# Performance work log

Hardware: AMD Instinct MI355X
Metric: run time of the kernel (lower is better)

The kernel has to match this reference:

```python
import jax, jax.numpy as jnp
import numpy as np

BN_EPS = 1e-5
DIST_EPS = 1e-8


def setup_inputs() -> dict:
    key = jax.random.key(0)
    ks = jax.random.split(key, 8)
    B, N, M = 8, 8192, 2048
    C1, C2 = 128, 256
    Cin = C1 + C2  # 384
    H = 256
    return {
        "xyz1": jax.random.normal(ks[0], (B, N, 3), dtype=jnp.float32),
        "xyz2": jax.random.normal(ks[1], (B, M, 3), dtype=jnp.float32),
        "points1": jax.random.normal(ks[2], (B, N, C1), dtype=jnp.float32),
        "points2": jax.random.normal(ks[3], (B, M, C2), dtype=jnp.float32),
        "W1": jax.random.normal(ks[4], (H, Cin), dtype=jnp.float32) * 0.05,
        "b1": jnp.zeros((H,), dtype=jnp.float32),
        "gamma1": jnp.ones((H,), dtype=jnp.float32),
        "beta1": jnp.zeros((H,), dtype=jnp.float32),
        "W2": jax.random.normal(ks[5], (H, H), dtype=jnp.float32) * 0.05,
        "b2": jnp.zeros((H,), dtype=jnp.float32),
        "gamma2": jnp.ones((H,), dtype=jnp.float32),
        "beta2": jnp.zeros((H,), dtype=jnp.float32),
    }


def _interpolate(xyz1, xyz2, points2):
    # squared distances (B,N,M) via the bmm expansion, as in square_distance
    d = (jnp.sum(xyz1 * xyz1, -1)[:, :, None]
         + jnp.sum(xyz2 * xyz2, -1)[:, None, :]
         - 2.0 * jnp.einsum("bnc,bmc->bnm", xyz1, xyz2))
    neg, idx = jax.lax.top_k(-d, 3)          # 3 smallest distances
    dists = -neg                              # (B,N,3)
    recip = 1.0 / (dists + DIST_EPS)
    w = recip / jnp.sum(recip, -1, keepdims=True)  # (B,N,3)
    gathered = jax.vmap(lambda p, i: p[i])(points2, idx)  # (B,N,3,C2)
    return jnp.einsum("bnkc,bnk->bnc", gathered, w)


def _conv_bn_relu(x, W, b, gamma, beta):
    # pointwise conv1d: (B,N,Cin) x (Cout,Cin) -> (B,N,Cout)
    y = jnp.einsum("bnc,oc->bno", x, W) + b
    mean = jnp.mean(y, axis=(0, 1))           # BatchNorm1d (training-mode batch stats)
    var = jnp.var(y, axis=(0, 1))
    y = (y - mean) * jax.lax.rsqrt(var + BN_EPS) * gamma + beta
    return jax.nn.relu(y)


def reference(xyz1, xyz2, points1, points2, W1, b1, gamma1, beta1, W2, b2, gamma2, beta2):
    interp = _interpolate(xyz1, xyz2, points2)          # (B,N,C2)
    x = jnp.concatenate([points1, interp], axis=-1)     # (B,N,C1+C2)
    x = _conv_bn_relu(x, W1, b1, gamma1, beta1)
    x = _conv_bn_relu(x, W2, b2, gamma2, beta2)
    return x  # (B,N,mlp[-1])
```

## Files before the change

kernel.cpp:

```cpp
#include <hip/hip_runtime.h>
#include <hip/hip_bf16.h>
#include <stdint.h>

#define B_SZ  8
#define N_Q   8192
#define M_PT  2048
#define C1    128
#define C2    256
#define CIN   384
#define H_OUT 256
#define R_TOT 65536

#define NCH   8
#define CHM   (M_PT / NCH)
#define QPB   32

typedef __bf16 bf16x8 __attribute__((ext_vector_type(8)));
typedef __bf16 bf16x4 __attribute__((ext_vector_type(4)));
typedef __bf16 bf16x2 __attribute__((ext_vector_type(2)));
typedef float  f32x4  __attribute__((ext_vector_type(4)));

__device__ __forceinline__ void async_copy16(const void* g, void* l) {
    __builtin_amdgcn_global_load_lds(
        (const __attribute__((address_space(1))) unsigned int*)g,
        (__attribute__((address_space(3))) unsigned int*)l,
        16, 0, 0);
}

__global__ __launch_bounds__(256) void f2bf2(const float* __restrict__ a, int na,
                                             const float* __restrict__ b, int nb,
                                             __bf16* __restrict__ oa,
                                             __bf16* __restrict__ ob) {
    int i = blockIdx.x * 256 + threadIdx.x;
    if (i < na)            oa[i] = (__bf16)a[i];
    else if (i - na < nb)  ob[i - na] = (__bf16)b[i - na];
}

__global__ __launch_bounds__(256) void knn_partial(
    const float* __restrict__ xyz1, const float* __restrict__ xyz2,
    float* __restrict__ cand_d, int* __restrict__ cand_i) {
    __shared__ float4 pos[CHM];

    const int tid = threadIdx.x;
    const int c   = blockIdx.x & (NCH - 1);
    const int qb  = (blockIdx.x >> 3) & 31;
    const int b   = blockIdx.x >> 8;

    {
        const float* x2 = xyz2 + ((size_t)b * M_PT + c * CHM) * 3;
        float x = x2[tid * 3], y = x2[tid * 3 + 1], z = x2[tid * 3 + 2];
        pos[tid] = make_float4(x, y, z, x * x + y * y + z * z);
    }
    __syncthreads();

    const int q = b * N_Q + qb * 256 + tid;
    const float* q1 = xyz1 + (size_t)q * 3;
    float x1 = q1[0], y1 = q1[1], z1 = q1[2];
    float n1 = x1 * x1 + y1 * y1 + z1 * z1;
    float d0 = 3.4e38f, d1 = 3.4e38f, d2 = 3.4e38f;
    int   i0 = 0, i1 = 0, i2 = 0;
    const int jb = c * CHM;
#pragma unroll 8
    for (int j = 0; j < CHM; ++j) {
        float4 p  = pos[j];
        float dot = fmaf(x1, p.x, fmaf(y1, p.y, z1 * p.z));
        float d   = fmaf(-2.f, dot, n1 + p.w);
        const int jj = jb + j;
        const bool c2 = d < d2, c1 = d < d1, c0 = d < d0;
        const int ni2 = c1 ? i1 : (c2 ? jj : i2);
        const int ni1 = c0 ? i0 : (c1 ? jj : i1);
        const int ni0 = c0 ? jj : i0;
        const float nd2 = fminf(fmaxf(d, d1), d2);
        const float nd1 = __builtin_amdgcn_fmed3f(d, d0, d1);
        const float nd0 = fminf(d, d0);
        i2 = ni2; i1 = ni1; i0 = ni0;
        d2 = nd2; d1 = nd1; d0 = nd0;
    }
    const size_t base = (size_t)q * (NCH * 3) + c * 3;
    cand_d[base] = d0; cand_d[base + 1] = d1; cand_d[base + 2] = d2;
    cand_i[base] = i0; cand_i[base + 1] = i1; cand_i[base + 2] = i2;
}

__global__ __launch_bounds__(256) void interp_gather(
    const float* __restrict__ p1,     const float* __restrict__ p2,
    const float* __restrict__ cand_d, const int* __restrict__ cand_i,
    __bf16* __restrict__ xb) {
    __shared__ float wgt[QPB * 3];
    __shared__ int   ids[QPB * 3];

    const int tid = threadIdx.x;
    const int b   = blockIdx.x >> 8;
    const int q0  = (blockIdx.x & 255) * QPB;

    if (tid < QPB) {
        const int q = b * N_Q + q0 + tid;
        const float* cd = cand_d + (size_t)q * (NCH * 3);
        const int*   ci = cand_i + (size_t)q * (NCH * 3);
        float d0 = 3.4e38f, d1 = 3.4e38f, d2 = 3.4e38f;
        int   i0 = 0, i1 = 0, i2 = 0;
#pragma unroll
        for (int t = 0; t < NCH * 3; ++t) {
            float d = cd[t]; int i = ci[t];
            const bool c2 = d < d2, c1 = d < d1, c0 = d < d0;
            const int ni2 = c1 ? i1 : (c2 ? i : i2);
            const int ni1 = c0 ? i0 : (c1 ? i : i1);
            const int ni0 = c0 ? i : i0;
            const float nd2 = fminf(fmaxf(d, d1), d2);
            const float nd1 = __builtin_amdgcn_fmed3f(d, d0, d1);
            const float nd0 = fminf(d, d0);
            i2 = ni2; i1 = ni1; i0 = ni0;
            d2 = nd2; d1 = nd1; d0 = nd0;
        }
        float r0 = 1.f / (d0 + 1e-8f), r1 = 1.f / (d1 + 1e-8f), r2 = 1.f / (d2 + 1e-8f);
        float rs = 1.f / (r0 + r1 + r2);
        wgt[tid * 3] = r0 * rs; wgt[tid * 3 + 1] = r1 * rs; wgt[tid * 3 + 2] = r2 * rs;
        ids[tid * 3] = i0;      ids[tid * 3 + 1] = i1;      ids[tid * 3 + 2] = i2;
    }
    __syncthreads();

    const int wave = tid >> 6, lane = tid & 63;
    const float* p2b = p2 + (size_t)b * M_PT * C2;
    const float* p1b = p1 + (size_t)(b * N_Q + q0) * C1;
    __bf16* outp = xb + (size_t)(b * N_Q + q0) * CIN;
    for (int qq = wave; qq < QPB; qq += 4) {
        float w0 = wgt[qq * 3], w1 = wgt[qq * 3 + 1], w2 = wgt[qq * 3 + 2];
        int   j0 = ids[qq * 3], j1 = ids[qq * 3 + 1], j2 = ids[qq * 3 + 2];
        const float4* ra = (const float4*)(p2b + (size_t)j0 * C2);
        const float4* rb = (const float4*)(p2b + (size_t)j1 * C2);
        const float4* rc = (const float4*)(p2b + (size_t)j2 * C2);
        float4 va = ra[lane], vb = rb[lane], vc = rc[lane];
        bf16x4 o;
        o[0] = (__bf16)(w0 * va.x + w1 * vb.x + w2 * vc.x);
        o[1] = (__bf16)(w0 * va.y + w1 * vb.y + w2 * vc.y);
        o[2] = (__bf16)(w0 * va.z + w1 * vb.z + w2 * vc.z);
        o[3] = (__bf16)(w0 * va.w + w1 * vb.w + w2 * vc.w);
        *(bf16x4*)(outp + (size_t)qq * CIN + C1 + lane * 4) = o;
        float2 pv = ((const float2*)(p1b + (size_t)qq * C1))[lane];
        bf16x2 o2; o2[0] = (__bf16)pv.x; o2[1] = (__bf16)pv.y;
        *(bf16x2*)(outp + (size_t)qq * CIN + lane * 2) = o2;
    }
}

template <int K, bool OUT_BF16>
__global__ __launch_bounds__(256, 2) void gemm_bt(const __bf16* __restrict__ A,
                                                  const __bf16* __restrict__ Bw,
                                                  void* __restrict__ Cout,
                                                  float* __restrict__ partS,
                                                  float* __restrict__ partQ) {
    __shared__ __attribute__((aligned(16))) __bf16 As[128 * 32];
    __shared__ __attribute__((aligned(16))) __bf16 Bs[128 * 32];
    const int tid  = threadIdx.x;
    const int wave = tid >> 6, lane = tid & 63;
    const int wm = wave >> 1, wn = wave & 1;
    const int quad = lane >> 4, r16 = lane & 15;
    const int bx = blockIdx.x & 1, by = blockIdx.x >> 1;
    const int l4 = lane >> 2, lk = (lane & 3) * 8;

    f32x4 acc[4][4] = {};

    const __bf16* gA = A  + (size_t)(by * 128 + wave * 32 + l4) * K + lk;
    const __bf16* gB = Bw + (size_t)(bx * 128 + wave * 32 + l4) * K + lk;
    char* lA = (char*)As + wave * 2048;
    char* lB = (char*)Bs + wave * 2048;

    for (int k0 = 0; k0 < K; k0 += 32) {
        async_copy16(gA + k0,                  lA);
        async_copy16(gA + k0 + (size_t)16 * K, lA + 1024);
        async_copy16(gB + k0,                  lB);
        async_copy16(gB + k0 + (size_t)16 * K, lB + 1024);
        __syncthreads();

        bf16x8 af[4], bf[4];
#pragma unroll
        for (int t = 0; t < 4; ++t)
            af[t] = *(const bf16x8*)(As + (wm * 64 + t * 16 + r16) * 32 + quad * 8);
#pragma unroll
        for (int u = 0; u < 4; ++u)
            bf[u] = *(const bf16x8*)(Bs + (wn * 64 + u * 16 + r16) * 32 + quad * 8);
#pragma unroll
        for (int t = 0; t < 4; ++t)
#pragma unroll
            for (int u = 0; u < 4; ++u)
                acc[t][u] = __builtin_amdgcn_mfma_f32_16x16x32_bf16(af[t], bf[u], acc[t][u], 0, 0, 0);
        __syncthreads();
    }

#pragma unroll
    for (int t = 0; t < 4; ++t) {
#pragma unroll
        for (int u = 0; u < 4; ++u) {
            const int col = bx * 128 + wn * 64 + u * 16 + r16;
#pragma unroll
            for (int r = 0; r < 4; ++r) {
                const int row = by * 128 + wm * 64 + t * 16 + quad * 4 + r;
                if (OUT_BF16)
                    ((__bf16*)Cout)[(size_t)row * H_OUT + col] = (__bf16)acc[t][u][r];
                else
                    ((float*)Cout)[(size_t)row * H_OUT + col] = acc[t][u][r];
            }
        }
    }

    float* redS = (float*)As;
    float* redQ = ((float*)As) + 1024;
    const int slot = wm * 4 + quad;
#pragma unroll
    for (int u = 0; u < 4; ++u) {
        float s = 0.f, qq = 0.f;
#pragma unroll
        for (int t = 0; t < 4; ++t)
#pragma unroll
            for (int r = 0; r < 4; ++r) { float v = acc[t][u][r]; s += v; qq = fmaf(v, v, qq); }
        const int col = wn * 64 + u * 16 + r16;
        redS[col * 8 + slot] = s;
        redQ[col * 8 + slot] = qq;
    }
    __syncthreads();
    if (tid < 128) {
        float s = 0.f, qq = 0.f;
#pragma unroll
        for (int k = 0; k < 8; ++k) { s += redS[tid * 8 + k]; qq += redQ[tid * 8 + k]; }
        partS[(size_t)blockIdx.x * 128 + tid] = s;
        partQ[(size_t)blockIdx.x * 128 + tid] = qq;
    }
}

__global__ __launch_bounds__(256) void bn_finalize(const float* __restrict__ pS,
                                                   const float* __restrict__ pQ,
                                                   const float* __restrict__ gamma,
                                                   const float* __restrict__ beta,
                                                   float* __restrict__ sc,
                                                   float* __restrict__ sh) {
    const int c = threadIdx.x;
    const int half = c >> 7, lo = c & 127;
    float s = 0.f, q = 0.f;
    for (int p = 0; p < 512; ++p) {
        const size_t off = (size_t)(p * 2 + half) * 128 + lo;
        s += pS[off];
        q += pQ[off];
    }
    const float inv = 1.f / (float)R_TOT;
    float mean = s * inv;
    float var  = q * inv - mean * mean;
    float a    = gamma[c] * rsqrtf(var + 1e-5f);
    sc[c] = a;
    sh[c] = beta[c] - mean * a;
}

__global__ __launch_bounds__(256) void apply_bf16(__bf16* __restrict__ y,
                                                  const float* __restrict__ sc,
                                                  const float* __restrict__ sh) {
    __shared__ float scs[256], shs[256];
    scs[threadIdx.x] = sc[threadIdx.x];
    shs[threadIdx.x] = sh[threadIdx.x];
    __syncthreads();
    size_t i = ((size_t)blockIdx.x * 256 + threadIdx.x) * 8;
    int c0 = (int)(i & 255);
    bf16x8 v = *(const bf16x8*)(y + i);
#pragma unroll
    for (int e = 0; e < 8; ++e) {
        float f = fmaf((float)v[e], scs[c0 + e], shs[c0 + e]);
        v[e] = (__bf16)fmaxf(f, 0.f);
    }
    *(bf16x8*)(y + i) = v;
}

__global__ __launch_bounds__(256) void apply_f32(float* __restrict__ y,
                                                 const float* __restrict__ sc,
                                                 const float* __restrict__ sh) {
    __shared__ float scs[256], shs[256];
    scs[threadIdx.x] = sc[threadIdx.x];
    shs[threadIdx.x] = sh[threadIdx.x];
    __syncthreads();
    size_t i = ((size_t)blockIdx.x * 256 + threadIdx.x) * 4;
    int c0 = (int)(i & 255);
    float4 v = *(const float4*)(y + i);
    v.x = fmaxf(fmaf(v.x, scs[c0 + 0], shs[c0 + 0]), 0.f);
    v.y = fmaxf(fmaf(v.y, scs[c0 + 1], shs[c0 + 1]), 0.f);
    v.z = fmaxf(fmaf(v.z, scs[c0 + 2], shs[c0 + 2]), 0.f);
    v.w = fmaxf(fmaf(v.w, scs[c0 + 3], shs[c0 + 3]), 0.f);
    *(float4*)(y + i) = v;
}

extern "C" void kernel_launch(void* const* d_in, const int* in_sizes, int n_in,
                              void* d_out, int out_size, void* d_ws, size_t ws_size,
                              hipStream_t stream) {
    const float* xyz1 = (const float*)d_in[0];
    const float* xyz2 = (const float*)d_in[1];
    const float* p1   = (const float*)d_in[2];
    const float* p2   = (const float*)d_in[3];
    const float* W1   = (const float*)d_in[4];
    const float* g1   = (const float*)d_in[6];
    const float* be1  = (const float*)d_in[7];
    const float* W2   = (const float*)d_in[8];
    const float* g2   = (const float*)d_in[10];
    const float* be2  = (const float*)d_in[11];
    float* out = (float*)d_out;

    char* ws = (char*)d_ws;
    __bf16* xb     = (__bf16*)(ws);
    __bf16* y1b    = (__bf16*)(ws + 50331648);
    float*  cand_d = (float*) (ws + 50331648);
    int*    cand_i = (int*)   (ws + 56623104);
    __bf16* wb1    = (__bf16*)(ws + 83886080);
    __bf16* wb2    = (__bf16*)(ws + 84082688);
    float*  sc1    = (float*) (ws + 84213760);
    float*  sh1    = sc1 + 256;
    float*  sc2    = sc1 + 512;
    float*  sh2    = sc1 + 768;

    float* partS1 = (float*)d_out;
    float* partQ1 = partS1 + 131072;
    float* partS2 = (float*)ws;
    float* partQ2 = partS2 + 131072;

    f2bf2<<<640, 256, 0, stream>>>(W1, H_OUT * CIN, W2, H_OUT * H_OUT, wb1, wb2);

    knn_partial<<<B_SZ * 32 * NCH, 256, 0, stream>>>(xyz1, xyz2, cand_d, cand_i);
    interp_gather<<<R_TOT / QPB, 256, 0, stream>>>(p1, p2, cand_d, cand_i, xb);

    gemm_bt<CIN, true><<<1024, 256, 0, stream>>>(xb, wb1, (void*)y1b, partS1, partQ1);
    bn_finalize<<<1, 256, 0, stream>>>(partS1, partQ1, g1, be1, sc1, sh1);
    apply_bf16<<<8192, 256, 0, stream>>>(y1b, sc1, sh1);

    gemm_bt<H_OUT, false><<<1024, 256, 0, stream>>>(y1b, wb2, (void*)out, partS2, partQ2);
    bn_finalize<<<1, 256, 0, stream>>>(partS2, partQ2, g2, be2, sc2, sh2);
    apply_f32<<<16384, 256, 0, stream>>>(out, sc2, sh2);
}
```

Baseline: 320.8 us.

## Split KNN into value-only top-3 pass, merge, and index-recovery pass; parallelize BN finalize

Replaces the single KNN pass that tracked distances and indices together with three kernels. The first keeps only the three smallest partial distances per chunk, dropping the query norm and using fmed3 with no index selects. A merge kernel then combines the chunks and computes the interpolation weights, and a second pass recomputes distances to recover indices by exact float equality. BN finalize also moves from a single-block serial loop to one block per channel with a tree reduction. The cost is a second full distance sweep, plus index recovery that relies on bitwise-identical recomputed distances and resolves ties to the lowest index.

```diff
diff --git a/kernel.cpp b/kernel.cpp
--- a/kernel.cpp
+++ b/kernel.cpp
@@ -36,54 +36,105 @@
     else if (i - na < nb)  ob[i - na] = (__bf16)b[i - na];
 }
 
-__global__ __launch_bounds__(256) void knn_partial(
+__global__ __launch_bounds__(256) void knn_vals(
     const float* __restrict__ xyz1, const float* __restrict__ xyz2,
-    float* __restrict__ cand_d, int* __restrict__ cand_i) {
+    float4* __restrict__ vals4) {
     __shared__ float4 pos[CHM];
-
     const int tid = threadIdx.x;
     const int c   = blockIdx.x & (NCH - 1);
     const int qb  = (blockIdx.x >> 3) & 31;
     const int b   = blockIdx.x >> 8;
-
     {
         const float* x2 = xyz2 + ((size_t)b * M_PT + c * CHM) * 3;
         float x = x2[tid * 3], y = x2[tid * 3 + 1], z = x2[tid * 3 + 2];
-        pos[tid] = make_float4(x, y, z, x * x + y * y + z * z);
+        pos[tid] = make_float4(-2.f * x, -2.f * y, -2.f * z,
+                               fmaf(x, x, fmaf(y, y, z * z)));
     }
     __syncthreads();
 
     const int q = b * N_Q + qb * 256 + tid;
     const float* q1 = xyz1 + (size_t)q * 3;
     float x1 = q1[0], y1 = q1[1], z1 = q1[2];
-    float n1 = x1 * x1 + y1 * y1 + z1 * z1;
-    float d0 = 3.4e38f, d1 = 3.4e38f, d2 = 3.4e38f;
-    int   i0 = 0, i1 = 0, i2 = 0;
-    const int jb = c * CHM;
+    float v0 = 3.4e38f, v1 = 3.4e38f, v2 = 3.4e38f;
 #pragma unroll 8
     for (int j = 0; j < CHM; ++j) {
-        float4 p  = pos[j];
-        float dot = fmaf(x1, p.x, fmaf(y1, p.y, z1 * p.z));
-        float d   = fmaf(-2.f, dot, n1 + p.w);
-        const int jj = jb + j;
-        const bool c2 = d < d2, c1 = d < d1, c0 = d < d0;
-        const int ni2 = c1 ? i1 : (c2 ? jj : i2);
-        const int ni1 = c0 ? i0 : (c1 ? jj : i1);
-        const int ni0 = c0 ? jj : i0;
-        const float nd2 = fminf(fmaxf(d, d1), d2);
-        const float nd1 = __builtin_amdgcn_fmed3f(d, d0, d1);
-        const float nd0 = fminf(d, d0);
-        i2 = ni2; i1 = ni1; i0 = ni0;
-        d2 = nd2; d1 = nd1; d0 = nd0;
-    }
-    const size_t base = (size_t)q * (NCH * 3) + c * 3;
-    cand_d[base] = d0; cand_d[base + 1] = d1; cand_d[base + 2] = d2;
-    cand_i[base] = i0; cand_i[base + 1] = i1; cand_i[base + 2] = i2;
+        float4 p = pos[j];
+        float d  = fmaf(p.x, x1, fmaf(p.y, y1, fmaf(p.z, z1, p.w)));
+        float n0 = fminf(d, v0);
+        float n1 = __builtin_amdgcn_fmed3f(d, v0, v1);
+        float n2 = __builtin_amdgcn_fmed3f(d, v1, v2);
+        v0 = n0; v1 = n1; v2 = n2;
+    }
+    vals4[(size_t)c * R_TOT + q] = make_float4(v0, v1, v2, 0.f);
+}
+
+__global__ __launch_bounds__(256) void knn_merge(
+    const float4* __restrict__ vals4, const float* __restrict__ xyz1,
+    float4* __restrict__ v4, float4* __restrict__ w4) {
+    const int q = blockIdx.x * 256 + threadIdx.x;
+    float v0 = 3.4e38f, v1 = 3.4e38f, v2 = 3.4e38f;
+#pragma unroll
+    for (int c = 0; c < NCH; ++c) {
+        float4 t = vals4[(size_t)c * R_TOT + q];
+#pragma unroll
+        for (int k = 0; k < 3; ++k) {
+            float d  = (k == 0) ? t.x : (k == 1) ? t.y : t.z;
+            float n0 = fminf(d, v0);
+            float n1 = __builtin_amdgcn_fmed3f(d, v0, v1);
+            float n2 = __builtin_amdgcn_fmed3f(d, v1, v2);
+            v0 = n0; v1 = n1; v2 = n2;
+        }
+    }
+    const float* q1 = xyz1 + (size_t)q * 3;
+    float x1 = q1[0], y1 = q1[1], z1 = q1[2];
+    float n1q = fmaf(x1, x1, fmaf(y1, y1, z1 * z1));
+    float r0 = 1.f / ((v0 + n1q) + 1e-8f);
+    float r1 = 1.f / ((v1 + n1q) + 1e-8f);
+    float r2 = 1.f / ((v2 + n1q) + 1e-8f);
+    float rs = 1.f / (r0 + r1 + r2);
+    v4[q] = make_float4(v0, v1, v2, 0.f);
+    w4[q] = make_float4(r0 * rs, r1 * rs, r2 * rs, 0.f);
+}
+
+__global__ __launch_bounds__(256) void knn_recover(
+    const float* __restrict__ xyz1, const float* __restrict__ xyz2,
+    const float4* __restrict__ v4, int4* __restrict__ ci4) {
+    __shared__ float4 pos[CHM];
+    const int tid = threadIdx.x;
+    const int c   = blockIdx.x & (NCH - 1);
+    const int qb  = (blockIdx.x >> 3) & 31;
+    const int b   = blockIdx.x >> 8;
+    {
+        const float* x2 = xyz2 + ((size_t)b * M_PT + c * CHM) * 3;
+        float x = x2[tid * 3], y = x2[tid * 3 + 1], z = x2[tid * 3 + 2];
+        pos[tid] = make_float4(-2.f * x, -2.f * y, -2.f * z,
+                               fmaf(x, x, fmaf(y, y, z * z)));
+    }
+    __syncthreads();
+
+    const int q = b * N_Q + qb * 256 + tid;
+    const float* q1 = xyz1 + (size_t)q * 3;
+    float x1 = q1[0], y1 = q1[1], z1 = q1[2];
+    const float4 vv = v4[q];
+    int i0 = 0x7fffffff, i1 = 0x7fffffff, i2 = 0x7fffffff;
+    const int jb = c * CHM;
+#pragma unroll 4
+    for (int j = 0; j < CHM; ++j) {
+        float4 p = pos[j];
+        float d  = fmaf(p.x, x1, fmaf(p.y, y1, fmaf(p.z, z1, p.w)));
+        if (d <= vv.z) {
+            const int jj = jb + j;
+            i0 = min(i0, (d == vv.x) ? jj : 0x7fffffff);
+            i1 = min(i1, (d == vv.y) ? jj : 0x7fffffff);
+            i2 = min(i2, (d == vv.z) ? jj : 0x7fffffff);
+        }
+    }
+    ci4[(size_t)c * R_TOT + q] = make_int4(i0, i1, i2, 0);
 }
 
 __global__ __launch_bounds__(256) void interp_gather(
-    const float* __restrict__ p1,     const float* __restrict__ p2,
-    const float* __restrict__ cand_d, const int* __restrict__ cand_i,
+    const float* __restrict__ p1,  const float* __restrict__ p2,
+    const int4* __restrict__ ci4,  const float4* __restrict__ w4,
     __bf16* __restrict__ xb) {
     __shared__ float wgt[QPB * 3];
     __shared__ int   ids[QPB * 3];
@@ -94,27 +145,15 @@
 
     if (tid < QPB) {
         const int q = b * N_Q + q0 + tid;
-        const float* cd = cand_d + (size_t)q * (NCH * 3);
-        const int*   ci = cand_i + (size_t)q * (NCH * 3);
-        float d0 = 3.4e38f, d1 = 3.4e38f, d2 = 3.4e38f;
-        int   i0 = 0, i1 = 0, i2 = 0;
-#pragma unroll
-        for (int t = 0; t < NCH * 3; ++t) {
-            float d = cd[t]; int i = ci[t];
-            const bool c2 = d < d2, c1 = d < d1, c0 = d < d0;
-            const int ni2 = c1 ? i1 : (c2 ? i : i2);
-            const int ni1 = c0 ? i0 : (c1 ? i : i1);
-            const int ni0 = c0 ? i : i0;
-            const float nd2 = fminf(fmaxf(d, d1), d2);
-            const float nd1 = __builtin_amdgcn_fmed3f(d, d0, d1);
-            const float nd0 = fminf(d, d0);
-            i2 = ni2; i1 = ni1; i0 = ni0;
-            d2 = nd2; d1 = nd1; d0 = nd0;
+        int i0 = 0x7fffffff, i1 = 0x7fffffff, i2 = 0x7fffffff;
+#pragma unroll
+        for (int c = 0; c < NCH; ++c) {
+            int4 t = ci4[(size_t)c * R_TOT + q];
+            i0 = min(i0, t.x); i1 = min(i1, t.y); i2 = min(i2, t.z);
         }
-        float r0 = 1.f / (d0 + 1e-8f), r1 = 1.f / (d1 + 1e-8f), r2 = 1.f / (d2 + 1e-8f);
-        float rs = 1.f / (r0 + r1 + r2);
-        wgt[tid * 3] = r0 * rs; wgt[tid * 3 + 1] = r1 * rs; wgt[tid * 3 + 2] = r2 * rs;
-        ids[tid * 3] = i0;      ids[tid * 3 + 1] = i1;      ids[tid * 3 + 2] = i2;
+        float4 w = w4[q];
+        wgt[tid * 3] = w.x; wgt[tid * 3 + 1] = w.y; wgt[tid * 3 + 2] = w.z;
+        ids[tid * 3] = i0;  ids[tid * 3 + 1] = i1;  ids[tid * 3 + 2] = i2;
     }
     __syncthreads();
 
@@ -231,20 +270,27 @@
                                                    const float* __restrict__ beta,
                                                    float* __restrict__ sc,
                                                    float* __restrict__ sh) {
-    const int c = threadIdx.x;
+    __shared__ float rs[256], rq[256];
+    const int c = blockIdx.x;
+    const int t = threadIdx.x;
     const int half = c >> 7, lo = c & 127;
-    float s = 0.f, q = 0.f;
-    for (int p = 0; p < 512; ++p) {
-        const size_t off = (size_t)(p * 2 + half) * 128 + lo;
-        s += pS[off];
-        q += pQ[off];
-    }
-    const float inv = 1.f / (float)R_TOT;
-    float mean = s * inv;
-    float var  = q * inv - mean * mean;
-    float a    = gamma[c] * rsqrtf(var + 1e-5f);
-    sc[c] = a;
-    sh[c] = beta[c] - mean * a;
+    const size_t o1 = (size_t)(2 * t + half) * 128 + lo;
+    const size_t o2 = (size_t)(2 * (t + 256) + half) * 128 + lo;
+    rs[t] = pS[o1] + pS[o2];
+    rq[t] = pQ[o1] + pQ[o2];
+    __syncthreads();
+    for (int k = 128; k > 0; k >>= 1) {
+        if (t < k) { rs[t] += rs[t + k]; rq[t] += rq[t + k]; }
+        __syncthreads();
+    }
+    if (t == 0) {
+        const float inv = 1.f / (float)R_TOT;
+        float mean = rs[0] * inv;
+        float var  = rq[0] * inv - mean * mean;
+        float a    = gamma[c] * rsqrtf(var + 1e-5f);
+        sc[c] = a;
+        sh[c] = beta[c] - mean * a;
+    }
 }
 
 __global__ __launch_bounds__(256) void apply_bf16(__bf16* __restrict__ y,
@@ -300,8 +346,10 @@
     char* ws = (char*)d_ws;
     __bf16* xb     = (__bf16*)(ws);
     __bf16* y1b    = (__bf16*)(ws + 50331648);
-    float*  cand_d = (float*) (ws + 50331648);
-    int*    cand_i = (int*)   (ws + 56623104);
+    float4* vals4  = (float4*)(ws + 50331648);
+    int4*   ci4    = (int4*)  (ws + 58720256);
+    float4* v4     = (float4*)(ws + 67108864);
+    float4* w4     = (float4*)(ws + 68157440);
     __bf16* wb1    = (__bf16*)(ws + 83886080);
     __bf16* wb2    = (__bf16*)(ws + 84082688);
     float*  sc1    = (float*) (ws + 84213760);
@@ -316,14 +364,16 @@
 
     f2bf2<<<640, 256, 0, stream>>>(W1, H_OUT * CIN, W2, H_OUT * H_OUT, wb1, wb2);
 
-    knn_partial<<<B_SZ * 32 * NCH, 256, 0, stream>>>(xyz1, xyz2, cand_d, cand_i);
-    interp_gather<<<R_TOT / QPB, 256, 0, stream>>>(p1, p2, cand_d, cand_i, xb);
+    knn_vals<<<B_SZ * 32 * NCH, 256, 0, stream>>>(xyz1, xyz2, vals4);
+    knn_merge<<<R_TOT / 256, 256, 0, stream>>>(vals4, xyz1, v4, w4);
+    knn_recover<<<B_SZ * 32 * NCH, 256, 0, stream>>>(xyz1, xyz2, v4, ci4);
+    interp_gather<<<R_TOT / QPB, 256, 0, stream>>>(p1, p2, ci4, w4, xb);
 
     gemm_bt<CIN, true><<<1024, 256, 0, stream>>>(xb, wb1, (void*)y1b, partS1, partQ1);
-    bn_finalize<<<1, 256, 0, stream>>>(partS1, partQ1, g1, be1, sc1, sh1);
+    bn_finalize<<<256, 256, 0, stream>>>(partS1, partQ1, g1, be1, sc1, sh1);
     apply_bf16<<<8192, 256, 0, stream>>>(y1b, sc1, sh1);
 
     gemm_bt<H_OUT, false><<<1024, 256, 0, stream>>>(y1b, wb2, (void*)out, partS2, partQ2);
-    bn_finalize<<<1, 256, 0, stream>>>(partS2, partQ2, g2, be2, sc2, sh2);
+    bn_finalize<<<256, 256, 0, stream>>>(partS2, partQ2, g2, be2, sc2, sh2);
     apply_f32<<<16384, 256, 0, stream>>>(out, sc2, sh2);
 }
```

Result: faster. 280.4 us (-12.6%).
